# Optimization experiments

Measured on AMD Instinct MI355X. Metric: run time of the kernel, lower is better.

Reference implementation:

```python
import jax, jax.numpy as jnp
import numpy as np

N_VEH = 8388608  # number of vehicles (rows)
N_FEAT = 8       # features per vehicle


def setup_inputs() -> dict:
    key = jax.random.key(0)
    k1, k2 = jax.random.split(key)
    out = jax.random.normal(k1, (N_VEH, N_FEAT), dtype=jnp.float32)
    target = jax.random.normal(k2, (N_VEH, N_FEAT), dtype=jnp.float32)
    x = jnp.zeros((1,), dtype=jnp.float32)  # unused by the loss, kept for signature fidelity
    return {"out": out, "target": target, "x": x}


def reference(out, target, x):
    # Handmade L1: sum over features per vehicle, sum over vehicles,
    # then divide by number of vehicles (rows) for reduction='mean'.
    # (Note: differs from torch L1Loss mean, which divides by total elements;
    # the module returns the handmade value, so we match that.)
    total = jnp.sum(jnp.abs(out - target))
    return total / out.shape[0]
```

## Files before the change

### kernel.cpp

```cpp
#include <hip/hip_runtime.h>


#define NBLOCKS 2048
#define NTHREADS 256

__global__ __launch_bounds__(NTHREADS) void l1_partial_kernel(
    const float4* __restrict__ a, const float4* __restrict__ b,
    float* __restrict__ partial, int n4) {
    int tid = blockIdx.x * NTHREADS + threadIdx.x;
    int stride = gridDim.x * NTHREADS;
    float s = 0.0f;
    for (int i = tid; i < n4; i += stride) {
        float4 x = a[i];
        float4 y = b[i];
        s += fabsf(x.x - y.x);
        s += fabsf(x.y - y.y);
        s += fabsf(x.z - y.z);
        s += fabsf(x.w - y.w);
    }
    #pragma unroll
    for (int off = 32; off > 0; off >>= 1)
        s += __shfl_down(s, off, 64);
    __shared__ float smem[NTHREADS / 64];
    int lane = threadIdx.x & 63;
    int wave = threadIdx.x >> 6;
    if (lane == 0) smem[wave] = s;
    __syncthreads();
    if (threadIdx.x == 0) {
        float t = 0.0f;
        #pragma unroll
        for (int w = 0; w < NTHREADS / 64; ++w) t += smem[w];
        partial[blockIdx.x] = t;
    }
}

__global__ __launch_bounds__(NTHREADS) void l1_final_kernel(
    const float* __restrict__ partial, float* __restrict__ out,
    int nblocks, float inv_n) {
    float s = 0.0f;
    for (int i = threadIdx.x; i < nblocks; i += NTHREADS)
        s += partial[i];
    #pragma unroll
    for (int off = 32; off > 0; off >>= 1)
        s += __shfl_down(s, off, 64);
    __shared__ double smem[NTHREADS / 64];
    int lane = threadIdx.x & 63;
    int wave = threadIdx.x >> 6;
    if (lane == 0) smem[wave] = (double)s;
    __syncthreads();
    if (threadIdx.x == 0) {
        double t = 0.0;
        #pragma unroll
        for (int w = 0; w < NTHREADS / 64; ++w) t += smem[w];
        out[0] = (float)(t * (double)inv_n);
    }
}

extern "C" void kernel_launch(void* const* d_in, const int* in_sizes, int n_in,
                              void* d_out, int out_size, void* d_ws, size_t ws_size,
                              hipStream_t stream) {
    const float* a = (const float*)d_in[0];
    const float* b = (const float*)d_in[1];
    float* out = (float*)d_out;
    float* partial = (float*)d_ws;

    int n = in_sizes[0];
    int n4 = n >> 2;
    int n_veh = n >> 3;
    float inv_n = 1.0f / (float)n_veh;

    l1_partial_kernel<<<NBLOCKS, NTHREADS, 0, stream>>>(
        (const float4*)a, (const float4*)b, partial, n4);
    l1_final_kernel<<<1, NTHREADS, 0, stream>>>(partial, out, NBLOCKS, inv_n);
}
```

Baseline: 503.3 us.

## Use one float4 per thread with a three-stage tree reduction

Replaces the fixed 2048-block grid-stride loop with a grid that assigns one float4 pair per thread, then reduces block partials through an extra intermediate kernel before the final sum. The aim is more memory-level parallelism and better bandwidth use on the large streaming read. In exchange it adds a third kernel launch, many more per-block reductions, and a larger workspace buffer. Stage 3 assumes the second-level count fits in a single block.

Result: faster. 489.0 us (-2.8%).

```diff
diff --git a/kernel.cpp b/kernel.cpp
--- a/kernel.cpp
+++ b/kernel.cpp
@@ -1,29 +1,25 @@
 #include <hip/hip_runtime.h>
 
 
-#define NBLOCKS 2048
 #define NTHREADS 256
 
-__global__ __launch_bounds__(NTHREADS) void l1_partial_kernel(
+__global__ __launch_bounds__(NTHREADS) void l1_stage1(
     const float4* __restrict__ a, const float4* __restrict__ b,
     float* __restrict__ partial, int n4) {
-    int tid = blockIdx.x * NTHREADS + threadIdx.x;
-    int stride = gridDim.x * NTHREADS;
+    const int tid = blockIdx.x * NTHREADS + threadIdx.x;
     float s = 0.0f;
-    for (int i = tid; i < n4; i += stride) {
-        float4 x = a[i];
-        float4 y = b[i];
-        s += fabsf(x.x - y.x);
-        s += fabsf(x.y - y.y);
-        s += fabsf(x.z - y.z);
-        s += fabsf(x.w - y.w);
+    if (tid < n4) {
+        float4 x = a[tid];
+        float4 y = b[tid];
+        s = fabsf(x.x - y.x) + fabsf(x.y - y.y) +
+            fabsf(x.z - y.z) + fabsf(x.w - y.w);
     }
     #pragma unroll
     for (int off = 32; off > 0; off >>= 1)
         s += __shfl_down(s, off, 64);
     __shared__ float smem[NTHREADS / 64];
-    int lane = threadIdx.x & 63;
-    int wave = threadIdx.x >> 6;
+    const int lane = threadIdx.x & 63;
+    const int wave = threadIdx.x >> 6;
     if (lane == 0) smem[wave] = s;
     __syncthreads();
     if (threadIdx.x == 0) {
@@ -34,18 +30,36 @@
     }
 }
 
-__global__ __launch_bounds__(NTHREADS) void l1_final_kernel(
-    const float* __restrict__ partial, float* __restrict__ out,
-    int nblocks, float inv_n) {
-    float s = 0.0f;
-    for (int i = threadIdx.x; i < nblocks; i += NTHREADS)
-        s += partial[i];
+__global__ __launch_bounds__(NTHREADS) void l1_stage2(
+    const float* __restrict__ in, float* __restrict__ outp, int count) {
+    const int tid = blockIdx.x * NTHREADS + threadIdx.x;
+    float s = (tid < count) ? in[tid] : 0.0f;
+    #pragma unroll
+    for (int off = 32; off > 0; off >>= 1)
+        s += __shfl_down(s, off, 64);
+    __shared__ float smem[NTHREADS / 64];
+    const int lane = threadIdx.x & 63;
+    const int wave = threadIdx.x >> 6;
+    if (lane == 0) smem[wave] = s;
+    __syncthreads();
+    if (threadIdx.x == 0) {
+        float t = 0.0f;
+        #pragma unroll
+        for (int w = 0; w < NTHREADS / 64; ++w) t += smem[w];
+        outp[blockIdx.x] = t;
+    }
+}
+
+__global__ __launch_bounds__(NTHREADS) void l1_stage3(
+    const float* __restrict__ in, float* __restrict__ out,
+    int count, float inv_n) {
+    float s = (threadIdx.x < count) ? in[threadIdx.x] : 0.0f;
     #pragma unroll
     for (int off = 32; off > 0; off >>= 1)
         s += __shfl_down(s, off, 64);
     __shared__ double smem[NTHREADS / 64];
-    int lane = threadIdx.x & 63;
-    int wave = threadIdx.x >> 6;
+    const int lane = threadIdx.x & 63;
+    const int wave = threadIdx.x >> 6;
     if (lane == 0) smem[wave] = (double)s;
     __syncthreads();
     if (threadIdx.x == 0) {
@@ -62,14 +76,19 @@
     const float* a = (const float*)d_in[0];
     const float* b = (const float*)d_in[1];
     float* out = (float*)d_out;
-    float* partial = (float*)d_ws;
 
     int n = in_sizes[0];
     int n4 = n >> 2;
     int n_veh = n >> 3;
     float inv_n = 1.0f / (float)n_veh;
 
-    l1_partial_kernel<<<NBLOCKS, NTHREADS, 0, stream>>>(
-        (const float4*)a, (const float4*)b, partial, n4);
-    l1_final_kernel<<<1, NTHREADS, 0, stream>>>(partial, out, NBLOCKS, inv_n);
+    int nb1 = (n4 + NTHREADS - 1) / NTHREADS;
+    int nb2 = (nb1 + NTHREADS - 1) / NTHREADS;
+
+    float* p1 = (float*)d_ws;
+    float* p2 = p1 + nb1;
+
+    l1_stage1<<<nb1, NTHREADS, 0, stream>>>((const float4*)a, (const float4*)b, p1, n4);
+    l1_stage2<<<nb2, NTHREADS, 0, stream>>>(p1, p2, nb1);
+    l1_stage3<<<1, NTHREADS, 0, stream>>>(p2, out, nb2, inv_n);
 }
```
